# Kernel tuning notes

Hardware: AMD Instinct MI355X
Metric: run time of the kernel (lower is better)

Reference implementation:

```python
import jax, jax.numpy as jnp
import numpy as np

B, N = 4, 8192
D = 128
DEPTH = 4
LEAF = 32
HEADS = 4
HD = D // HEADS
SLOTS = 24
RANKS = [20, 32, 52, 82]                      # rank at encoder step j (fine -> coarse)
EXP = [RANKS[j] * (2 ** j) for j in range(DEPTH)]  # HODLR head output dims


def _rope_tables(seq_len, dim):
    inv_freq = 1.0 / (10000.0 ** (jnp.arange(0, dim, 2, dtype=jnp.float32) / dim))
    t = jnp.arange(seq_len, dtype=jnp.float32)
    freqs = t[:, None] * inv_freq[None, :]
    emb = jnp.concatenate([freqs, freqs], axis=-1)   # [S, dim]
    return jnp.cos(emb), jnp.sin(emb)


def _rotate_half(x):
    x1, x2 = jnp.split(x, 2, axis=-1)
    return jnp.concatenate([-x2, x1], axis=-1)


def _layernorm(x, g, b, eps=1e-5):
    mu = jnp.mean(x, -1, keepdims=True)
    var = jnp.mean((x - mu) ** 2, -1, keepdims=True)
    return (x - mu) * jax.lax.rsqrt(var + eps) * g + b


def _block_attn(h, qkv_w, qkv_b, pw, pb, cos, sin):
    Bc, Nc, C = h.shape
    nb = Nc // LEAF
    xb = h.reshape(Bc * nb, LEAF, C)
    qkv = (xb @ qkv_w + qkv_b).reshape(Bc * nb, LEAF, 3, HEADS, HD)
    qkv = qkv.transpose(2, 0, 3, 1, 4)               # [3, BN, H, L, hd]
    q, k, v = qkv[0], qkv[1], qkv[2]
    q = q * cos + _rotate_half(q) * sin              # full-dim RoPE (rope_dim == head_dim)
    k = k * cos + _rotate_half(k) * sin
    attn = jax.nn.softmax(jnp.einsum('bhqd,bhkd->bhqk', q, k) * (HD ** -0.5), axis=-1)
    o = jnp.einsum('bhqk,bhkd->bhqd', attn, v).transpose(0, 2, 1, 3).reshape(Bc * nb, LEAF, C)
    return (o @ pw + pb).reshape(Bc, Nc, C)


def _forward(x, cen_w, cen_b, nbr_w, nbr_b, inp_w, inp_b,
             leafp_w, leafp_b, leafh_w, leafh_b, log_scale_leaf,
             ln1_g, ln1_b, qkv_w, qkv_b, attnp_w, attnp_b,
             ln2_g, ln2_b, mlp1_w, mlp1_b, mlp2_w, mlp2_b, ds_w, ds_b,
             hu_w0, hu_b0, hv_w0, hv_b0, hu_w1, hu_b1, hv_w1, hv_b1,
             hu_w2, hu_b2, hv_w2, hv_b2, hu_w3, hu_b3, hv_w3, hv_b3):
    Bx, Nx, _ = x.shape
    # --- SymmetricNeighborEmbed (24 neighbor slots, vectorized) ---
    pos_i = x[..., 0:3]
    diag_i = x[..., 3:4]
    h_center = jnp.concatenate([pos_i, diag_i], -1) @ cen_w + cen_b          # [B,N,D]
    nb_feat = x[..., 4:4 + 5 * SLOTS].reshape(Bx, Nx, SLOTS, 5)
    rel = nb_feat[..., 0:1]
    pos_j = nb_feat[..., 1:4]
    w_ij = nb_feat[..., 4:5]
    active = (w_ij != 0.0).astype(x.dtype)
    feat = jnp.concatenate([rel * active, (pos_j - pos_i[:, :, None, :]) * active, w_ij], -1)
    e = (feat @ nbr_w + nbr_b) * active                                       # [B,N,24,D]
    h = h_center + jnp.sum(e, axis=2)
    h = h @ inp_w + inp_b
    # --- leaf dense diagonal blocks ---
    nl = Nx // LEAF
    hl = h.reshape(Bx, nl, LEAF, D) @ leafp_w + leafp_b                       # [B,nl,32,32]
    u_leaf = hl @ leafh_w + leafh_b
    dense = jnp.einsum('blik,bljk->blij', u_leaf, u_leaf) * jnp.exp(log_scale_leaf)
    diag_a = x[..., 3]                                                        # scale_A defaults to 1.0
    mask = jnp.abs(diag_a) > 1e-6
    new_diag = jnp.where(mask, 1.0 / jnp.where(mask, diag_a, 1.0), 1.0).reshape(Bx, nl, LEAF)
    dense = dense + new_diag[..., :, None] * jnp.eye(LEAF, dtype=x.dtype)
    # --- down-only encoder: transformer block -> HODLR head -> 2:1 downsample ---
    cos, sin = _rope_tables(LEAF, HD)
    hu = [(hu_w0, hu_b0), (hu_w1, hu_b1), (hu_w2, hu_b2), (hu_w3, hu_b3)]
    hv = [(hv_w0, hv_b0), (hv_w1, hv_b1), (hv_w2, hv_b2), (hv_w3, hv_b3)]
    us, vs = [], []
    for j in range(DEPTH):
        a = _block_attn(_layernorm(h, ln1_g[j], ln1_b[j]),
                        qkv_w[j], qkv_b[j], attnp_w[j], attnp_b[j], cos, sin)
        h = h + a
        m = _layernorm(h, ln2_g[j], ln2_b[j])
        m = jax.nn.gelu(m @ mlp1_w[j] + mlp1_b[j], approximate=False) @ mlp2_w[j] + mlp2_b[j]
        h = h + m
        us.append((h @ hu[j][0] + hu[j][1]).reshape(Bx, Nx, RANKS[j]))
        vs.append((h @ hv[j][0] + hv[j][1]).reshape(Bx, Nx, RANKS[j]))
        Bh, n, c = h.shape
        h = h.reshape(Bh, n // 2, 2 * c) @ ds_w[j] + ds_b[j]
    # single flat output: dense leaf blocks + all U/V HODLR factors
    return jnp.concatenate([dense.reshape(Bx, -1),
                            jnp.concatenate(us, -1).reshape(Bx, -1),
                            jnp.concatenate(vs, -1).reshape(Bx, -1)], -1)


def setup_inputs():
    key = jax.random.key(0)
    ks = iter(jax.random.split(key, 64))
    def rn(shape, s=0.05):
        return jax.random.normal(next(ks), shape, jnp.float32) * s
    z = lambda *s: jnp.zeros(s, jnp.float32)
    o = lambda *s: jnp.ones(s, jnp.float32)
    inp = {
        'x': jax.random.normal(next(ks), (B, N, 4 + 5 * SLOTS), jnp.float32),
        'cen_w': rn((4, D)), 'cen_b': z(D),
        'nbr_w': rn((5, D)), 'nbr_b': z(D),
        'inp_w': rn((D, D)), 'inp_b': z(D),
        'leafp_w': rn((D, LEAF)), 'leafp_b': z(LEAF),
        'leafh_w': rn((LEAF, LEAF), 0.01), 'leafh_b': z(LEAF),
        'log_scale_leaf': jnp.full((1,), np.log(0.01), jnp.float32),
        'ln1_g': o(DEPTH, D), 'ln1_b': z(DEPTH, D),
        'qkv_w': rn((DEPTH, D, 3 * D)), 'qkv_b': z(DEPTH, 3 * D),
        'attnp_w': rn((DEPTH, D, D)), 'attnp_b': z(DEPTH, D),
        'ln2_g': o(DEPTH, D), 'ln2_b': z(DEPTH, D),
        'mlp1_w': rn((DEPTH, D, 4 * D)), 'mlp1_b': z(DEPTH, 4 * D),
        'mlp2_w': rn((DEPTH, 4 * D, D)), 'mlp2_b': z(DEPTH, D),
        'ds_w': rn((DEPTH, 2 * D, D)), 'ds_b': z(DEPTH, D),
    }
    for j in range(DEPTH):
        inp['hu_w%d' % j] = rn((D, EXP[j]), 0.01)
        inp['hu_b%d' % j] = z(EXP[j])
        inp['hv_w%d' % j] = rn((D, EXP[j]), 0.01)
        inp['hv_b%d' % j] = z(EXP[j])
    return inp


def reference(x, cen_w, cen_b, nbr_w, nbr_b, inp_w, inp_b,
              leafp_w, leafp_b, leafh_w, leafh_b, log_scale_leaf,
              ln1_g, ln1_b, qkv_w, qkv_b, attnp_w, attnp_b,
              ln2_g, ln2_b, mlp1_w, mlp1_b, mlp2_w, mlp2_b, ds_w, ds_b,
              hu_w0, hu_b0, hv_w0, hv_b0, hu_w1, hu_b1, hv_w1, hv_b1,
              hu_w2, hu_b2, hv_w2, hv_b2, hu_w3, hu_b3, hv_w3, hv_b3):
    return _forward(x, cen_w, cen_b, nbr_w, nbr_b, inp_w, inp_b,
                    leafp_w, leafp_b, leafh_w, leafh_b, log_scale_leaf,
                    ln1_g, ln1_b, qkv_w, qkv_b, attnp_w, attnp_b,
                    ln2_g, ln2_b, mlp1_w, mlp1_b, mlp2_w, mlp2_b, ds_w, ds_b,
                    hu_w0, hu_b0, hv_w0, hv_b0, hu_w1, hu_b1, hv_w1, hv_b1,
                    hu_w2, hu_b2, hv_w2, hv_b2, hu_w3, hu_b3, hv_w3, hv_b3)
```

## Files before the change

kernel.cpp:

```cpp
#include <hip/hip_runtime.h>
#include <math.h>

#define DEV __device__ __forceinline__

constexpr int XFv = 124;
constexpr size_t OPB   = 3309568;
constexpr size_t UBASE = 262144;
constexpr size_t VBASE = 1785856;
constexpr int UVWID = 186;

using bfrag  = __attribute__((ext_vector_type(8))) short;
using f32x4v = __attribute__((ext_vector_type(4))) float;

DEV float* at4p(float* base, int t, int c0, int W) {
  return base + t * W + ((c0 + 4 * t) & (W - 1));
}
DEV float& at1r(float* base, int t, int c, int W) {
  return base[t * W + (((c & ~3) + 4 * t) & (W - 1)) + (c & 3)];
}
DEV float4 ld4g(const float* p) { return *(const float4*)p; }
DEV void fma4(float4& a, float s, const float4& w) {
  a.x += s * w.x; a.y += s * w.y; a.z += s * w.z; a.w += s * w.w;
}
DEV float gelu_fast(float x) {
// ... 157 lines not shown
  int t = tid & 31, cg = tid >> 5;
  {
    float4 acc = ld4g(&lpb[4 * cg]);
    for (int k4 = 0; k4 < 128; k4 += 4) {
      float4 xv = *(const float4*)at4p(HS, t, k4, 128);
      float xa[4] = {xv.x, xv.y, xv.z, xv.w};
#pragma unroll
      for (int kk = 0; kk < 4; kk++)
        fma4(acc, xa[kk], ld4g(&lpw[(k4 + kk) * 32 + 4 * cg]));
    }
    *(float4*)at4p(HL, t, 4 * cg, 32) = acc;
  }
  __syncthreads();
  {
    float4 acc = ld4g(&lhb[4 * cg]);
    for (int k4 = 0; k4 < 32; k4 += 4) {
      float4 xv = *(const float4*)at4p(HL, t, k4, 32);
      float xa[4] = {xv.x, xv.y, xv.z, xv.w};
#pragma unroll
      for (int kk = 0; kk < 4; kk++)
        fma4(acc, xa[kk], ld4g(&lhw[(k4 + kk) * 32 + 4 * cg]));
    }
    *(float4*)at4p(UL, t, 4 * cg, 32) = acc;
  }
  __syncthreads();
  {
    float scale = expf(lsc[0]);
    float acc[4] = {0.f, 0.f, 0.f, 0.f};
    for (int k4 = 0; k4 < 32; k4 += 4) {
      float4 xv = *(const float4*)at4p(UL, t, k4, 32);
      float xa[4] = {xv.x, xv.y, xv.z, xv.w};
#pragma unroll
      for (int kk = 0; kk < 4; kk++) {
        int k = k4 + kk;
#pragma unroll
        for (int i2 = 0; i2 < 4; i2++)
          acc[i2] += xa[kk] * at1r(UL, 4 * cg + i2, k, 32);
      }
    }
    int b = leaf >> 8, l = leaf & 255;
#pragma unroll
    for (int i2 = 0; i2 < 4; i2++) {
      int c = 4 * cg + i2;
      float v = acc[i2] * scale;
      if (c == t) {
        float dg = x[(size_t)(leaf * 32 + t) * XFv + 3];
        v += (fabsf(dg) > 1e-6f) ? (1.0f / dg) : 1.0f;
      }
      out[(size_t)b * OPB + (size_t)l * 1024 + t * 32 + c] = v;
    }
  }
}

__global__ __launch_bounds__(256, 4) void layer_mfma_kernel(
    float* __restrict__ h,
    const float* __restrict__ lng, const float* __restrict__ lnb,
    const ushort* __restrict__ wqkvt, const float* __restrict__ bqkv,
    const ushort* __restrict__ wpt, const float* __restrict__ pb,
    const float* __restrict__ rt,
    const float* __restrict__ ln2g, const float* __restrict__ ln2b,
    const ushort* __restrict__ w1t, const float* __restrict__ b1,
    const ushort* __restrict__ w2t, const float* __restrict__ b2) {
  __shared__ __align__(16) ushort SM[16384];
  ushort* XN = SM;
  ushort* QB = SM + 4096;
  ushort* KB = SM + 8192;
  ushort* VT = SM + 12288;
  float*  HS = (float*)(SM + 8192);
  int tid = threadIdx.x;
  size_t base = (size_t)blockIdx.x * (32 * 128);

  {
    int m = tid >> 3, p = tid & 7;
    const float* row = h + base + m * 128 + p * 16;
    float v[16];
    float s = 0.f;
#pragma unroll
    for (int i = 0; i < 16; i += 4) {
      float4 t4 = ld4g(row + i);
      v[i] = t4.x; v[i + 1] = t4.y; v[i + 2] = t4.z; v[i + 3] = t4.w;
      s += t4.x + t4.y + t4.z + t4.w;
    }
    s += __shfl_xor(s, 1); s += __shfl_xor(s, 2); s += __shfl_xor(s, 4);
    float mu = s * (1.0f / 128.0f);
    float s2 = 0.f;
#pragma unroll
    for (int i = 0; i < 16; i++) { float d = v[i] - mu; s2 += d * d; }
    s2 += __shfl_xor(s2, 1); s2 += __shfl_xor(s2, 2); s2 += __shfl_xor(s2, 4);
    float rs = rsqrtf(s2 * (1.0f / 128.0f) + 1e-5f);
    unsigned* XW = (unsigned*)XN;
#pragma unroll
    for (int i = 0; i < 16; i += 2) {
      int c = p * 16 + i;
      float x0 = (v[i] - mu) * rs * lng[c] + lnb[c];
      float x1 = (v[i + 1] - mu) * rs * lng[c + 1] + lnb[c + 1];
      int kp = c >> 1;
      XW[m * 64 + ((kp + 4 * m) & 63)] =
          (unsigned)f2bf(x0) | ((unsigned)f2bf(x1) << 16);
    }
  }
  __syncthreads();

  int w = tid >> 6, l = tid & 63, lm = l & 15, q = l >> 4;

  {
    f32x4v acc[2][6];
#pragma unroll
    for (int mt = 0; mt < 2; mt++)
#pragma unroll
      for (int nt = 0; nt < 6; nt++) acc[mt][nt] = (f32x4v){0.f, 0.f, 0.f, 0.f};
    for (int ks = 0; ks < 4; ks++) {
      bfrag a[2];
#pragma unroll
      for (int mt = 0; mt < 2; mt++) {
        int mm = mt * 16 + lm;
// ... 96 lines not shown
          int qt = mt2 * 16 + q * 4 + r;
          int kc = nt2 * 16 + lm;
          SP[head * 1024 + qt * 32 + (((kc & ~7) + 8 * qt) & 31) + (kc & 7)] =
              f2bf(sc[mt2][nt2][r] * scl);
        }
  }
  __syncthreads();

  {
    if (tid < 128) {
      int head = tid >> 5, qt = tid & 31;
      ushort* rowp = SP + head * 1024 + qt * 32;
      float v[32];
#pragma unroll
      for (int pc = 0; pc < 4; pc++) {
        uint4 ch = *(const uint4*)&rowp[pc * 8];
        unsigned uu[4] = {ch.x, ch.y, ch.z, ch.w};
#pragma unroll
        for (int i2 = 0; i2 < 4; i2++) {
          v[pc * 8 + 2 * i2]     = __uint_as_float(uu[i2] << 16);
          v[pc * 8 + 2 * i2 + 1] = __uint_as_float(uu[i2] & 0xffff0000u);
        }
      }
      float mx = -1e30f;
#pragma unroll
      for (int i = 0; i < 32; i++) mx = fmaxf(mx, v[i]);
      float s = 0.f;
#pragma unroll
      for (int i = 0; i < 32; i++) { v[i] = __expf(v[i] - mx); s += v[i]; }
      float inv = 1.0f / s;
#pragma unroll
      for (int pc = 0; pc < 4; pc++) {
        uint4 ch;
        unsigned uu[4];
#pragma unroll
        for (int i2 = 0; i2 < 4; i2++)
          uu[i2] = (unsigned)f2bf(v[pc * 8 + 2 * i2] * inv) |
                   ((unsigned)f2bf(v[pc * 8 + 2 * i2 + 1] * inv) << 16);
        ch.x = uu[0]; ch.y = uu[1]; ch.z = uu[2]; ch.w = uu[3];
        *(uint4*)&rowp[pc * 8] = ch;
      }
    }
  }
  __syncthreads();

  ushort* OB = QB;
  {
    int head = w;
    f32x4v ov[2][2];
#pragma unroll
    for (int a2 = 0; a2 < 2; a2++)
#pragma unroll
      for (int b2 = 0; b2 < 2; b2++) ov[a2][b2] = (f32x4v){0.f, 0.f, 0.f, 0.f};
    bfrag pa[2], vb[2];
#pragma unroll
    for (int mt2 = 0; mt2 < 2; mt2++) {
      int qt = mt2 * 16 + lm;
      pa[mt2] = *(const bfrag*)&SP[head * 1024 + qt * 32 + ((q * 8 + 8 * qt) & 31)];
    }
#pragma unroll
    for (int nt2 = 0; nt2 < 2; nt2++) {
      int gdim = head * 32 + nt2 * 16 + lm;
      vb[nt2] = *(const bfrag*)&VT[gdim * 32 + ((q * 8 + 8 * gdim) & 31)];
    }
#pragma unroll
    for (int mt2 = 0; mt2 < 2; mt2++)
#pragma unroll
      for (int nt2 = 0; nt2 < 2; nt2++)
        ov[mt2][nt2] = __builtin_amdgcn_mfma_f32_16x16x32_bf16(
            pa[mt2], vb[nt2], ov[mt2][nt2], 0, 0, 0);
#pragma unroll
    for (int mt2 = 0; mt2 < 2; mt2++)
#pragma unroll
      for (int nt2 = 0; nt2 < 2; nt2++)
#pragma unroll
        for (int r = 0; r < 4; r++) {
          int qt = mt2 * 16 + q * 4 + r;
          int gdim = head * 32 + nt2 * 16 + lm;
          stb128(OB, qt, gdim, ov[mt2][nt2][r]);
        }
  }
  __syncthreads();

  {
    f32x4v po[2][2];
#pragma unroll
    for (int mt = 0; mt < 2; mt++)
#pragma unroll
      for (int nt = 0; nt < 2; nt++) po[mt][nt] = (f32x4v){0.f, 0.f, 0.f, 0.f};
    for (int ks = 0; ks < 4; ks++) {
      bfrag a[2];
#pragma unroll
      for (int mt = 0; mt < 2; mt++) {
        int mm = mt * 16 + lm;
        a[mt] = *(const bfrag*)&OB[mm * 128 + ((ks * 32 + q * 8 + 8 * mm) & 127)];
      }
#pragma unroll
      for (int nt = 0; nt < 2; nt++) {
        int n = w * 32 + nt * 16 + lm;
        bfrag b = *(const bfrag*)&wpt[(size_t)n * 128 + ks * 32 + q * 8];
#pragma unroll
        for (int mt = 0; mt < 2; mt++)
          po[mt][nt] = __builtin_amdgcn_mfma_f32_16x16x32_bf16(
              a[mt], b, po[mt][nt], 0, 0, 0);
      }
    }
#pragma unroll
    for (int nt = 0; nt < 2; nt++) {
      int n = w * 32 + nt * 16 + lm;
      float bv = pb[n];
#pragma unroll
      for (int mt = 0; mt < 2; mt++)
#pragma unroll
        for (int r = 0; r < 4; r++) {
          int mm = mt * 16 + q * 4 + r;
          at1r(HS, mm, n, 128) = po[mt][nt][r] + bv;
        }
    }
  }
  __syncthreads();

  {
    int j = tid & 31;
// ... 58 lines not shown
      for (int nt = 0; nt < 2; nt++) {
        int n = hc * 128 + w * 32 + nt * 16 + lm;
        bfrag b = *(const bfrag*)&w1t[(size_t)n * 128 + ks * 32 + q * 8];
#pragma unroll
        for (int mt = 0; mt < 2; mt++)
          acc1[mt][nt] = __builtin_amdgcn_mfma_f32_16x16x32_bf16(
              a[mt], b, acc1[mt][nt], 0, 0, 0);
      }
    }
    if (hc) __syncthreads();
#pragma unroll
    for (int nt = 0; nt < 2; nt++) {
      int nl = w * 32 + nt * 16 + lm;
      float b1v = b1[hc * 128 + nl];
#pragma unroll
      for (int mt = 0; mt < 2; mt++)
#pragma unroll
        for (int r = 0; r < 4; r++) {
          int mm = mt * 16 + q * 4 + r;
          float val = gelu_fast(acc1[mt][nt][r] + b1v);
          HC[mm * 128 + (((nl & ~7) + 8 * mm) & 127) + (nl & 7)] = f2bf(val);
        }
    }
    __syncthreads();
#pragma unroll
    for (int ks = 0; ks < 4; ks++) {
      bfrag a[2];
#pragma unroll
      for (int mt = 0; mt < 2; mt++) {
        int mm = mt * 16 + lm;
        a[mt] = *(const bfrag*)&HC[mm * 128 + ((ks * 32 + q * 8 + 8 * mm) & 127)];
      }
#pragma unroll
      for (int nt = 0; nt < 2; nt++) {
        int n = w * 32 + nt * 16 + lm;
        bfrag b = *(const bfrag*)&w2t[(size_t)n * 512 + hc * 128 + ks * 32 + q * 8];
#pragma unroll
        for (int mt = 0; mt < 2; mt++)
          acc2[mt][nt] = __builtin_amdgcn_mfma_f32_16x16x32_bf16(
              a[mt], b, acc2[mt][nt], 0, 0, 0);
      }
    }
  }

#pragma unroll
  for (int nt = 0; nt < 2; nt++) {
    int n = w * 32 + nt * 16 + lm;
    float b2v = b2[n];
#pragma unroll
    for (int mt = 0; mt < 2; mt++)
#pragma unroll
      for (int r = 0; r < 4; r++) {
        int mm = mt * 16 + q * 4 + r;
        h[base + (size_t)mm * 128 + n] = at1r(HS, mm, n, 128) + acc2[mt][nt][r] + b2v;
      }
  }
}

template <int EXPJ, int RANK, int LVL, int NSPLIT>
__global__ __launch_bounds__(256) void uv_mfma_kernel(
    const float* __restrict__ h,
    const ushort* __restrict__ uwt, const float* __restrict__ ub,
    const ushort* __restrict__ vwt, const float* __restrict__ vb,
    float* __restrict__ out, int Nj) {
  constexpr int NT16 = (EXPJ + 15) / 16;
  constexpr int NJOBS = 2 * NT16;
  constexpr int COFF = (LVL == 0) ? 0 : (LVL == 1) ? 20 : (LVL == 2) ? 52 : 104;
  __shared__ __align__(16) ushort XN[64 * 128];
  int tid = threadIdx.x;
  int t0 = blockIdx.x * 64;
  size_t base = (size_t)t0 * 128;
  {
    int m = tid >> 2, p = tid & 3;
    const float* row = h + base + m * 128 + p * 32;
    unsigned* XW = (unsigned*)XN;
#pragma unroll
    for (int i = 0; i < 32; i += 4) {
      float4 t4 = ld4g(row + i);
      int kp = (p * 32 + i) >> 1;
      XW[m * 64 + ((kp + 4 * m) & 63)] =
          (unsigned)f2bf(t4.x) | ((unsigned)f2bf(t4.y) << 16);
      XW[m * 64 + ((kp + 1 + 4 * m) & 63)] =
          (unsigned)f2bf(t4.z) | ((unsigned)f2bf(t4.w) << 16);
    }
  }
  __syncthreads();
  int bidx = t0 / Nj;
  int tl0 = t0 - bidx * Nj;
  size_t obase = (size_t)bidx * OPB;
  int w = tid >> 6, l = tid & 63, lm = l & 15, q = l >> 4;
  int gw = w + 4 * blockIdx.y;
  for (int jj = gw; jj < NJOBS; jj += 4 * NSPLIT) {
    int uvsel = jj & 1, nt = jj >> 1;
    const ushort* wt = uvsel ? vwt : uwt;
    const float* bias = uvsel ? vb : ub;
    size_t ob = obase + (uvsel ? VBASE : UBASE);
    f32x4v acc[4];
#pragma unroll
    for (int mt = 0; mt < 4; mt++) acc[mt] = (f32x4v){0.f, 0.f, 0.f, 0.f};
    for (int ks = 0; ks < 4; ks++) {
      bfrag b = *(const bfrag*)&wt[(size_t)(nt * 16 + lm) * 128 + ks * 32 + q * 8];
#pragma unroll
      for (int mt = 0; mt < 4; mt++) {
        int mm = mt * 16 + lm;
        int ke = ks * 32 + q * 8;
        bfrag a = *(const bfrag*)&XN[mm * 128 + ((ke + 8 * mm) & 127)];
        acc[mt] = __builtin_amdgcn_mfma_f32_16x16x32_bf16(a, b, acc[mt], 0, 0, 0);
      }
    }
    int c = nt * 16 + lm;
    if (c < EXPJ) {
      float bv = bias[c];
      int cdiv = c / RANK, cmod = c - cdiv * RANK;
#pragma unroll
      for (int mt = 0; mt < 4; mt++)
#pragma unroll
        for (int r = 0; r < 4; r++) {
          int mm = mt * 16 + q * 4 + r;
          int nrow = ((tl0 + mm) << LVL) + cdiv;
          out[ob + (size_t)nrow * UVWID + COFF + cmod] = acc[mt][r] + bv;
        }
    }
  }
}

__global__ __launch_bounds__(256) void ds_mfma_kernel(
    const float* __restrict__ hin, float* __restrict__ hout,
    const ushort* __restrict__ wt, const float* __restrict__ bias) {
  __shared__ __align__(16) ushort XN[64 * 256];
  int tid = threadIdx.x;
  size_t base = (size_t)blockIdx.x * (64 * 256);
  {
    int m = tid >> 2, p = tid & 3;
    const float* row = hin + base + m * 256 + p * 64;
    unsigned* XW = (unsigned*)XN;
#pragma unroll
    for (int i = 0; i < 64; i += 4) {
      float4 t4 = ld4g(row + i);
      int kp = (p * 64 + i) >> 1;
      XW[m * 128 + ((kp + 4 * m) & 127)] =
          (unsigned)f2bf(t4.x) | ((unsigned)f2bf(t4.y) << 16);
      XW[m * 128 + ((kp + 1 + 4 * m) & 127)] =
          (unsigned)f2bf(t4.z) | ((unsigned)f2bf(t4.w) << 16);
    }
  }
  __syncthreads();
  int w = tid >> 6, l = tid & 63, lm = l & 15, q = l >> 4;
  f32x4v acc[4][2];
#pragma unroll
  for (int mt = 0; mt < 4; mt++)
#pragma unroll
    for (int nt = 0; nt < 2; nt++) acc[mt][nt] = (f32x4v){0.f, 0.f, 0.f, 0.f};
  for (int ks = 0; ks < 8; ks++) {
    bfrag a[4];
#pragma unroll
    for (int mt = 0; mt < 4; mt++) {
      int mm = mt * 16 + lm;
      a[mt] = *(const bfrag*)&XN[mm * 256 + ((ks * 32 + q * 8 + 8 * mm) & 255)];
    }
#pragma unroll
    for (int nt = 0; nt < 2; nt++) {
      int n = w * 32 + nt * 16 + lm;
      bfrag b = *(const bfrag*)&wt[(size_t)n * 256 + ks * 32 + q * 8];
#pragma unroll
      for (int mt = 0; mt < 4; mt++)
        acc[mt][nt] = __builtin_amdgcn_mfma_f32_16x16x32_bf16(
            a[mt], b, acc[mt][nt], 0, 0, 0);
    }
  }
  size_t obase = (size_t)blockIdx.x * (64 * 128);
#pragma unroll
  for (int nt = 0; nt < 2; nt++) {
    int n = w * 32 + nt * 16 + lm;
    float bv = bias[n];
#pragma unroll
    for (int mt = 0; mt < 4; mt++)
#pragma unroll
      for (int r = 0; r < 4; r++) {
        int mm = mt * 16 + q * 4 + r;
        hout[obase + (size_t)mm * 128 + n] = acc[mt][nt][r] + bv;
      }
  }
}

extern "C" void kernel_launch(void* const* d_in, const int* in_sizes, int n_in,
                              void* d_out, int out_size, void* d_ws, size_t ws_size,
                              hipStream_t stream) {
  const float* x       = (const float*)d_in[0];
  const float* cen_w   = (const float*)d_in[1];
  const float* cen_b   = (const float*)d_in[2];
  const float* nbr_w   = (const float*)d_in[3];
  const float* nbr_b   = (const float*)d_in[4];
  const float* inp_w   = (const float*)d_in[5];
  const float* inp_b   = (const float*)d_in[6];
  const float* leafp_w = (const float*)d_in[7];
  const float* leafp_b = (const float*)d_in[8];
  const float* leafh_w = (const float*)d_in[9];
  const float* leafh_b = (const float*)d_in[10];
  const float* lscale  = (const float*)d_in[11];
  const float* ln1_g   = (const float*)d_in[12];
  const float* ln1_b   = (const float*)d_in[13];
  const float* qkv_w   = (const float*)d_in[14];
  const float* qkv_b   = (const float*)d_in[15];
  const float* attnp_w = (const float*)d_in[16];
  const float* attnp_b = (const float*)d_in[17];
  const float* ln2_g   = (const float*)d_in[18];
  const float* ln2_b   = (const float*)d_in[19];
  const float* mlp1_w  = (const float*)d_in[20];
  const float* mlp1_b  = (const float*)d_in[21];
  const float* mlp2_w  = (const float*)d_in[22];
  const float* mlp2_b  = (const float*)d_in[23];
  const float* ds_w    = (const float*)d_in[24];
  const float* ds_b    = (const float*)d_in[25];
  const float* huw[4], *hub[4], *hvw[4], *hvb[4];
  for (int j = 0; j < 4; j++) {
    huw[j] = (const float*)d_in[26 + 4 * j];
    hub[j] = (const float*)d_in[27 + 4 * j];
    hvw[j] = (const float*)d_in[28 + 4 * j];
    hvb[j] = (const float*)d_in[29 + 4 * j];
  }
  float* out = (float*)d_out;
  float* hA = (float*)d_ws;
  float* hB = hA + (size_t)4 * 8192 * 128;
  ushort* w1t = (ushort*)(hB + (size_t)2097152);
  ushort* w2t = w1t + (size_t)4 * 65536;
  ushort* uvt = w2t + (size_t)4 * 65536;
  const int NPAD[4] = {32, 64, 208, 656};
  ushort* uwt[4]; ushort* vwt[4];
  ushort* p = uvt;
  for (int j = 0; j < 4; j++) {
    uwt[j] = p; p += (size_t)NPAD[j] * 128;
    vwt[j] = p; p += (size_t)NPAD[j] * 128;
  }
  ushort* wqkvt = p;
  ushort* wpt   = wqkvt + (size_t)4 * 384 * 128;
  ushort* dswt  = wpt + (size_t)4 * 128 * 128;
  float* weff   = (float*)(dswt + (size_t)4 * 128 * 256);
  float* ropetab = weff + 1408;
  const int EXPJ_[4] = {20, 64, 208, 656};

  weff_prep_kernel<<<1, 128, 0, stream>>>(
      cen_w, cen_b, nbr_w, nbr_b, inp_w, inp_b, weff, ropetab);
  wprep_all_kernel<<<dim3(2, 8, 4), 256, 0, stream>>>(mlp1_w, w1t, 128, 512);
  wprep_all_kernel<<<dim3(8, 2, 4), 256, 0, stream>>>(mlp2_w, w2t, 512, 128);
  wprep_all_kernel<<<dim3(2, 6, 4), 256, 0, stream>>>(qkv_w, wqkvt, 128, 384);
  wprep_all_kernel<<<dim3(2, 2, 4), 256, 0, stream>>>(attnp_w, wpt, 128, 128);
  wprep_all_kernel<<<dim3(4, 2, 4), 256, 0, stream>>>(ds_w, dswt, 256, 128);
  {
    UVDesc d;
    for (int j = 0; j < 4; j++) {
      d.src[2 * j] = huw[j];     d.dst[2 * j] = uwt[j];
      d.src[2 * j + 1] = hvw[j]; d.dst[2 * j + 1] = vwt[j];
      d.expj[2 * j] = EXPJ_[j];  d.expj[2 * j + 1] = EXPJ_[j];
      d.npad[2 * j] = NPAD[j];   d.npad[2 * j + 1] = NPAD[j];
    }
    uvprep_all_kernel<<<dim3(328, 8), 256, 0, stream>>>(d);
  }

  node_embed2_kernel<<<(4 * 8192) / 64, 256, 0, stream>>>(x, weff, hA);
  leaf_dense_kernel<<<(4 * 8192) / 32, 256, 0, stream>>>(
      hA, x, leafp_w, leafp_b, leafh_w, leafh_b, lscale, out);

  float* cur = hA;
  float* nxt = hB;
  int Nj = 8192;
  for (int j = 0; j < 4; j++) {
    int tokens = 4 * Nj;
    layer_mfma_kernel<<<tokens / 32, 256, 0, stream>>>(
        cur, ln1_g + j * 128, ln1_b + j * 128,
        wqkvt + (size_t)j * 49152, qkv_b + j * 384,
        wpt + (size_t)j * 16384, attnp_b + j * 128, ropetab,
        ln2_g + j * 128, ln2_b + j * 128,
        w1t + (size_t)j * 65536, mlp1_b + j * 512,
        w2t + (size_t)j * 65536, mlp2_b + j * 128);
    if (j == 0)
      uv_mfma_kernel<20, 20, 0, 1><<<dim3(tokens / 64, 1), 256, 0, stream>>>(
          cur, uwt[0], hub[0], vwt[0], hvb[0], out, Nj);
    else if (j == 1)
      uv_mfma_kernel<64, 32, 1, 2><<<dim3(tokens / 64, 2), 256, 0, stream>>>(
          cur, uwt[1], hub[1], vwt[1], hvb[1], out, Nj);
    else if (j == 2)
      uv_mfma_kernel<208, 52, 2, 4><<<dim3(tokens / 64, 4), 256, 0, stream>>>(
          cur, uwt[2], hub[2], vwt[2], hvb[2], out, Nj);
    else
      uv_mfma_kernel<656, 82, 3, 8><<<dim3(tokens / 64, 8), 256, 0, stream>>>(
          cur, uwt[3], hub[3], vwt[3], hvb[3], out, Nj);
    ds_mfma_kernel<<<tokens / 128, 256, 0, stream>>>(
        cur, nxt, dswt + (size_t)j * 32768, ds_b + j * 128);
    float* tmp = cur; cur = nxt; nxt = tmp;
    Nj >>= 1;
  }
  (void)in_sizes; (void)n_in; (void)out_size; (void)ws_size;
}
```

Baseline: 444.2 us.

## Fuse HODLR U/V heads and downsample into per-level layer kernel

Merges the per-level U/V head projection and the downsample GEMM into the end of the transformer layer kernel. The layer output stays in shared memory, is converted to bf16 there, and feeds both projections, so the global write and re-read of h and two extra launches per level go away. Launch bounds move from 4 to 5 blocks per SM. The cost is that the last level's 656-wide U/V work is now spread over only 128 blocks with four waves each, which may leave the GPU underused, and the higher occupancy target may cause register spills.

```diff
diff --git a/kernel.cpp b/kernel.cpp
--- a/kernel.cpp
+++ b/kernel.cpp
@@ -233,15 +233,20 @@
   }
 }
 
-__global__ __launch_bounds__(256, 4) void layer_mfma_kernel(
-    float* __restrict__ h,
+template <int EXPJ, int RANK, int LVL>
+__global__ __launch_bounds__(256, 5) void layer_mfma_kernel(
+    const float* __restrict__ h, float* __restrict__ hout,
     const float* __restrict__ lng, const float* __restrict__ lnb,
     const ushort* __restrict__ wqkvt, const float* __restrict__ bqkv,
     const ushort* __restrict__ wpt, const float* __restrict__ pb,
     const float* __restrict__ rt,
     const float* __restrict__ ln2g, const float* __restrict__ ln2b,
     const ushort* __restrict__ w1t, const float* __restrict__ b1,
-    const ushort* __restrict__ w2t, const float* __restrict__ b2) {
+    const ushort* __restrict__ w2t, const float* __restrict__ b2,
+    const ushort* __restrict__ uwt, const float* __restrict__ ub,
+    const ushort* __restrict__ vwt, const float* __restrict__ vb,
+    float* __restrict__ out, int Nj,
+    const ushort* __restrict__ dwt, const float* __restrict__ dsb) {
   __shared__ __align__(16) ushort SM[16384];
   ushort* XN = SM;
   ushort* QB = SM + 4096;
@@ -444,7 +449,7 @@
     for (int a2 = 0; a2 < 2; a2++)
 #pragma unroll
       for (int b2 = 0; b2 < 2; b2++) ov[a2][b2] = (f32x4v){0.f, 0.f, 0.f, 0.f};
-    bfrag pa[2], vb[2];
+    bfrag pa[2], vb2[2];
 #pragma unroll
     for (int mt2 = 0; mt2 < 2; mt2++) {
       int qt = mt2 * 16 + lm;
@@ -453,14 +458,14 @@
 #pragma unroll
     for (int nt2 = 0; nt2 < 2; nt2++) {
       int gdim = head * 32 + nt2 * 16 + lm;
-      vb[nt2] = *(const bfrag*)&VT[gdim * 32 + ((q * 8 + 8 * gdim) & 31)];
+      vb2[nt2] = *(const bfrag*)&VT[gdim * 32 + ((q * 8 + 8 * gdim) & 31)];
     }
 #pragma unroll
     for (int mt2 = 0; mt2 < 2; mt2++)
 #pragma unroll
       for (int nt2 = 0; nt2 < 2; nt2++)
         ov[mt2][nt2] = __builtin_amdgcn_mfma_f32_16x16x32_bf16(
-            pa[mt2], vb[nt2], ov[mt2][nt2], 0, 0, 0);
+            pa[mt2], vb2[nt2], ov[mt2][nt2], 0, 0, 0);
 #pragma unroll
     for (int mt2 = 0; mt2 < 2; mt2++)
 #pragma unroll
@@ -625,134 +630,96 @@
 #pragma unroll
       for (int r = 0; r < 4; r++) {
         int mm = mt * 16 + q * 4 + r;
-        h[base + (size_t)mm * 128 + n] = at1r(HS, mm, n, 128) + acc2[mt][nt][r] + b2v;
-      }
-  }
-}
-
-template <int EXPJ, int RANK, int LVL, int NSPLIT>
-__global__ __launch_bounds__(256) void uv_mfma_kernel(
-    const float* __restrict__ h,
-    const ushort* __restrict__ uwt, const float* __restrict__ ub,
-    const ushort* __restrict__ vwt, const float* __restrict__ vb,
-    float* __restrict__ out, int Nj) {
-  constexpr int NT16 = (EXPJ + 15) / 16;
-  constexpr int NJOBS = 2 * NT16;
-  constexpr int COFF = (LVL == 0) ? 0 : (LVL == 1) ? 20 : (LVL == 2) ? 52 : 104;
-  __shared__ __align__(16) ushort XN[64 * 128];
-  int tid = threadIdx.x;
-  int t0 = blockIdx.x * 64;
-  size_t base = (size_t)t0 * 128;
-  {
-    int m = tid >> 2, p = tid & 3;
-    const float* row = h + base + m * 128 + p * 32;
+        at1r(HS, mm, n, 128) += acc2[mt][nt][r] + b2v;
+      }
+  }
+  __syncthreads();
+
+  {
+    int j = tid & 31;
     unsigned* XW = (unsigned*)XN;
 #pragma unroll
-    for (int i = 0; i < 32; i += 4) {
-      float4 t4 = ld4g(row + i);
-      int kp = (p * 32 + i) >> 1;
-      XW[m * 64 + ((kp + 4 * m) & 63)] =
-          (unsigned)f2bf(t4.x) | ((unsigned)f2bf(t4.y) << 16);
-      XW[m * 64 + ((kp + 1 + 4 * m) & 63)] =
-          (unsigned)f2bf(t4.z) | ((unsigned)f2bf(t4.w) << 16);
-    }
-  }
-  __syncthreads();
-  int bidx = t0 / Nj;
-  int tl0 = t0 - bidx * Nj;
-  size_t obase = (size_t)bidx * OPB;
-  int w = tid >> 6, l = tid & 63, lm = l & 15, q = l >> 4;
-  int gw = w + 4 * blockIdx.y;
-  for (int jj = gw; jj < NJOBS; jj += 4 * NSPLIT) {
-    int uvsel = jj & 1, nt = jj >> 1;
-    const ushort* wt = uvsel ? vwt : uwt;
-    const float* bias = uvsel ? vb : ub;
-    size_t ob = obase + (uvsel ? VBASE : UBASE);
-    f32x4v acc[4];
-#pragma unroll
-    for (int mt = 0; mt < 4; mt++) acc[mt] = (f32x4v){0.f, 0.f, 0.f, 0.f};
-    for (int ks = 0; ks < 4; ks++) {
-      bfrag b = *(const bfrag*)&wt[(size_t)(nt * 16 + lm) * 128 + ks * 32 + q * 8];
-#pragma unroll
-      for (int mt = 0; mt < 4; mt++) {
-        int mm = mt * 16 + lm;
-        int ke = ks * 32 + q * 8;
-        bfrag a = *(const bfrag*)&XN[mm * 128 + ((ke + 8 * mm) & 127)];
-        acc[mt] = __builtin_amdgcn_mfma_f32_16x16x32_bf16(a, b, acc[mt], 0, 0, 0);
-      }
-    }
-    int c = nt * 16 + lm;
-    if (c < EXPJ) {
-      float bv = bias[c];
-      int cdiv = c / RANK, cmod = c - cdiv * RANK;
-#pragma unroll
-      for (int mt = 0; mt < 4; mt++)
-#pragma unroll
-        for (int r = 0; r < 4; r++) {
-          int mm = mt * 16 + q * 4 + r;
-          int nrow = ((tl0 + mm) << LVL) + cdiv;
-          out[ob + (size_t)nrow * UVWID + COFF + cmod] = acc[mt][r] + bv;
+    for (int k2 = 0; k2 < 4; k2++) {
+      int idx = tid + 256 * k2;
+      int tok = idx >> 5;
+      float4 hv = *(const float4*)at4p(HS, tok, 4 * j, 128);
+      int kp = 2 * j;
+      XW[tok * 64 + ((kp + 4 * tok) & 63)] =
+          (unsigned)f2bf(hv.x) | ((unsigned)f2bf(hv.y) << 16);
+      XW[tok * 64 + ((kp + 1 + 4 * tok) & 63)] =
+          (unsigned)f2bf(hv.z) | ((unsigned)f2bf(hv.w) << 16);
+    }
+  }
+  __syncthreads();
+
+  {
+    constexpr int NT16 = (EXPJ + 15) / 16;
+    constexpr int NJOBS = 2 * NT16;
+    constexpr int COFF = (LVL == 0) ? 0 : (LVL == 1) ? 20 : (LVL == 2) ? 52 : 104;
+    int t0 = blockIdx.x * 32;
+    int bidx = t0 / Nj;
+    int tl0 = t0 - bidx * Nj;
+    size_t obase = (size_t)bidx * OPB;
+    for (int jj = w; jj < NJOBS; jj += 4) {
+      int uvsel = jj & 1, nt = jj >> 1;
+      const ushort* wt = uvsel ? vwt : uwt;
+      const float* bias = uvsel ? vb : ub;
+      size_t ob = obase + (uvsel ? VBASE : UBASE);
+      f32x4v acc[2];
+      acc[0] = (f32x4v){0.f, 0.f, 0.f, 0.f};
+      acc[1] = (f32x4v){0.f, 0.f, 0.f, 0.f};
+      for (int ks = 0; ks < 4; ks++) {
+        bfrag b = *(const bfrag*)&wt[(size_t)(nt * 16 + lm) * 128 + ks * 32 + q * 8];
+#pragma unroll
+        for (int mt = 0; mt < 2; mt++) {
+          int mm = mt * 16 + lm;
+          int ke = ks * 32 + q * 8;
+          bfrag a = *(const bfrag*)&XN[mm * 128 + ((ke + 8 * mm) & 127)];
+          acc[mt] = __builtin_amdgcn_mfma_f32_16x16x32_bf16(a, b, acc[mt], 0, 0, 0);
         }
-    }
-  }
-}
-
-__global__ __launch_bounds__(256) void ds_mfma_kernel(
-    const float* __restrict__ hin, float* __restrict__ hout,
-    const ushort* __restrict__ wt, const float* __restrict__ bias) {
-  __shared__ __align__(16) ushort XN[64 * 256];
-  int tid = threadIdx.x;
-  size_t base = (size_t)blockIdx.x * (64 * 256);
-  {
-    int m = tid >> 2, p = tid & 3;
-    const float* row = hin + base + m * 256 + p * 64;
-    unsigned* XW = (unsigned*)XN;
-#pragma unroll
-    for (int i = 0; i < 64; i += 4) {
-      float4 t4 = ld4g(row + i);
-      int kp = (p * 64 + i) >> 1;
-      XW[m * 128 + ((kp + 4 * m) & 127)] =
-          (unsigned)f2bf(t4.x) | ((unsigned)f2bf(t4.y) << 16);
-      XW[m * 128 + ((kp + 1 + 4 * m) & 127)] =
-          (unsigned)f2bf(t4.z) | ((unsigned)f2bf(t4.w) << 16);
-    }
-  }
-  __syncthreads();
-  int w = tid >> 6, l = tid & 63, lm = l & 15, q = l >> 4;
-  f32x4v acc[4][2];
-#pragma unroll
-  for (int mt = 0; mt < 4; mt++)
-#pragma unroll
-    for (int nt = 0; nt < 2; nt++) acc[mt][nt] = (f32x4v){0.f, 0.f, 0.f, 0.f};
-  for (int ks = 0; ks < 8; ks++) {
-    bfrag a[4];
-#pragma unroll
-    for (int mt = 0; mt < 4; mt++) {
-      int mm = mt * 16 + lm;
-      a[mt] = *(const bfrag*)&XN[mm * 256 + ((ks * 32 + q * 8 + 8 * mm) & 255)];
-    }
+      }
+      int c = nt * 16 + lm;
+      if (c < EXPJ) {
+        float bv = bias[c];
+        int cdiv = c / RANK, cmod = c - cdiv * RANK;
+#pragma unroll
+        for (int mt = 0; mt < 2; mt++)
+#pragma unroll
+          for (int r = 0; r < 4; r++) {
+            int mm = mt * 16 + q * 4 + r;
+            int nrow = ((tl0 + mm) << LVL) + cdiv;
+            out[ob + (size_t)nrow * UVWID + COFF + cmod] = acc[mt][r] + bv;
+          }
+      }
+    }
+  }
+
+  if constexpr (LVL < 3) {
+    f32x4v dacc[2];
+    dacc[0] = (f32x4v){0.f, 0.f, 0.f, 0.f};
+    dacc[1] = (f32x4v){0.f, 0.f, 0.f, 0.f};
+    for (int ks = 0; ks < 8; ks++) {
+      int mm = 2 * lm + (ks >> 2);
+      int col = (ks & 3) * 32 + q * 8;
+      bfrag a = *(const bfrag*)&XN[mm * 128 + ((col + 8 * mm) & 127)];
+#pragma unroll
+      for (int nt = 0; nt < 2; nt++) {
+        int n = w * 32 + nt * 16 + lm;
+        bfrag b = *(const bfrag*)&dwt[(size_t)n * 256 + ks * 32 + q * 8];
+        dacc[nt] = __builtin_amdgcn_mfma_f32_16x16x32_bf16(a, b, dacc[nt], 0, 0, 0);
+      }
+    }
+    size_t obase2 = (size_t)blockIdx.x * (16 * 128);
 #pragma unroll
     for (int nt = 0; nt < 2; nt++) {
       int n = w * 32 + nt * 16 + lm;
-      bfrag b = *(const bfrag*)&wt[(size_t)n * 256 + ks * 32 + q * 8];
-#pragma unroll
-      for (int mt = 0; mt < 4; mt++)
-        acc[mt][nt] = __builtin_amdgcn_mfma_f32_16x16x32_bf16(
-            a[mt], b, acc[mt][nt], 0, 0, 0);
-    }
-  }
-  size_t obase = (size_t)blockIdx.x * (64 * 128);
-#pragma unroll
-  for (int nt = 0; nt < 2; nt++) {
-    int n = w * 32 + nt * 16 + lm;
-    float bv = bias[n];
-#pragma unroll
-    for (int mt = 0; mt < 4; mt++)
+      float bv = dsb[n];
 #pragma unroll
       for (int r = 0; r < 4; r++) {
-        int mm = mt * 16 + q * 4 + r;
-        hout[obase + (size_t)mm * 128 + n] = acc[mt][nt][r] + bv;
-      }
+        int mm = q * 4 + r;
+        hout[obase2 + (size_t)mm * 128 + n] = dacc[nt][r] + bv;
+      }
+    }
   }
 }
 
@@ -836,32 +803,27 @@
 
   float* cur = hA;
   float* nxt = hB;
-  int Nj = 8192;
-  for (int j = 0; j < 4; j++) {
-    int tokens = 4 * Nj;
-    layer_mfma_kernel<<<tokens / 32, 256, 0, stream>>>(
-        cur, ln1_g + j * 128, ln1_b + j * 128,
-        wqkvt + (size_t)j * 49152, qkv_b + j * 384,
-        wpt + (size_t)j * 16384, attnp_b + j * 128, ropetab,
-        ln2_g + j * 128, ln2_b + j * 128,
-        w1t + (size_t)j * 65536, mlp1_b + j * 512,
-        w2t + (size_t)j * 65536, mlp2_b + j * 128);
-    if (j == 0)
-      uv_mfma_kernel<20, 20, 0, 1><<<dim3(tokens / 64, 1), 256, 0, stream>>>(
-          cur, uwt[0], hub[0], vwt[0], hvb[0], out, Nj);
-    else if (j == 1)
-      uv_mfma_kernel<64, 32, 1, 2><<<dim3(tokens / 64, 2), 256, 0, stream>>>(
-          cur, uwt[1], hub[1], vwt[1], hvb[1], out, Nj);
-    else if (j == 2)
-      uv_mfma_kernel<208, 52, 2, 4><<<dim3(tokens / 64, 4), 256, 0, stream>>>(
-          cur, uwt[2], hub[2], vwt[2], hvb[2], out, Nj);
-    else
-      uv_mfma_kernel<656, 82, 3, 8><<<dim3(tokens / 64, 8), 256, 0, stream>>>(
-          cur, uwt[3], hub[3], vwt[3], hvb[3], out, Nj);
-    ds_mfma_kernel<<<tokens / 128, 256, 0, stream>>>(
-        cur, nxt, dswt + (size_t)j * 32768, ds_b + j * 128);
-    float* tmp = cur; cur = nxt; nxt = tmp;
-    Nj >>= 1;
-  }
+  layer_mfma_kernel<20, 20, 0><<<32768 / 32, 256, 0, stream>>>(
+      cur, nxt, ln1_g, ln1_b, wqkvt, qkv_b, wpt, attnp_b, ropetab,
+      ln2_g, ln2_b, w1t, mlp1_b, w2t, mlp2_b,
+      uwt[0], hub[0], vwt[0], hvb[0], out, 8192, dswt, ds_b);
+  layer_mfma_kernel<64, 32, 1><<<16384 / 32, 256, 0, stream>>>(
+      nxt, cur, ln1_g + 128, ln1_b + 128, wqkvt + 49152, qkv_b + 384,
+      wpt + 16384, attnp_b + 128, ropetab,
+      ln2_g + 128, ln2_b + 128, w1t + 65536, mlp1_b + 512,
+      w2t + 65536, mlp2_b + 128,
+      uwt[1], hub[1], vwt[1], hvb[1], out, 4096, dswt + 32768, ds_b + 128);
+  layer_mfma_kernel<208, 52, 2><<<8192 / 32, 256, 0, stream>>>(
+      cur, nxt, ln1_g + 256, ln1_b + 256, wqkvt + 98304, qkv_b + 768,
+      wpt + 32768, attnp_b + 256, ropetab,
+      ln2_g + 256, ln2_b + 256, w1t + 131072, mlp1_b + 1024,
+      w2t + 131072, mlp2_b + 256,
+      uwt[2], hub[2], vwt[2], hvb[2], out, 2048, dswt + 65536, ds_b + 256);
+  layer_mfma_kernel<656, 82, 3><<<4096 / 32, 256, 0, stream>>>(
+      nxt, cur, ln1_g + 384, ln1_b + 384, wqkvt + 147456, qkv_b + 1152,
+      wpt + 49152, attnp_b + 384, ropetab,
+      ln2_g + 384, ln2_b + 384, w1t + 196608, mlp1_b + 1536,
+      w2t + 196608, mlp2_b + 384,
+      uwt[3], hub[3], vwt[3], hvb[3], out, 1024, dswt + 98304, ds_b + 384);
   (void)in_sizes; (void)n_in; (void)out_size; (void)ws_size;
 }
```

New measurement: 478.8 us. +7.8%, slower.

## Fuse downsample into UV head kernel and stage UV outputs for coalesced assembly

Applied to the files above, without the earlier changes.

Merges the downsample GEMM into the UV-projection kernel, so each block reuses the bf16 activation tile already in shared memory and one launch per level goes away. UV outputs now go to contiguous per-level staging buffers instead of scattered strided writes into the output. A final assemble kernel gathers them into the interleaved output layout with float2 stores. This adds an extra write and read of all UV data plus one more launch, in exchange for coalesced stores and fewer launches. The last level still issues a DS kernel argument but skips the downsample via constexpr.

```diff
diff --git a/kernel.cpp b/kernel.cpp
--- a/kernel.cpp
+++ b/kernel.cpp
@@ -444,7 +444,7 @@
     for (int a2 = 0; a2 < 2; a2++)
 #pragma unroll
       for (int b2 = 0; b2 < 2; b2++) ov[a2][b2] = (f32x4v){0.f, 0.f, 0.f, 0.f};
-    bfrag pa[2], vb[2];
+    bfrag pa[2], vb2[2];
 #pragma unroll
     for (int mt2 = 0; mt2 < 2; mt2++) {
       int qt = mt2 * 16 + lm;
@@ -453,14 +453,14 @@
 #pragma unroll
     for (int nt2 = 0; nt2 < 2; nt2++) {
       int gdim = head * 32 + nt2 * 16 + lm;
-      vb[nt2] = *(const bfrag*)&VT[gdim * 32 + ((q * 8 + 8 * gdim) & 31)];
+      vb2[nt2] = *(const bfrag*)&VT[gdim * 32 + ((q * 8 + 8 * gdim) & 31)];
     }
 #pragma unroll
     for (int mt2 = 0; mt2 < 2; mt2++)
 #pragma unroll
       for (int nt2 = 0; nt2 < 2; nt2++)
         ov[mt2][nt2] = __builtin_amdgcn_mfma_f32_16x16x32_bf16(
-            pa[mt2], vb[nt2], ov[mt2][nt2], 0, 0, 0);
+            pa[mt2], vb2[nt2], ov[mt2][nt2], 0, 0, 0);
 #pragma unroll
     for (int mt2 = 0; mt2 < 2; mt2++)
 #pragma unroll
@@ -631,14 +631,15 @@
 }
 
 template <int EXPJ, int RANK, int LVL, int NSPLIT>
-__global__ __launch_bounds__(256) void uv_mfma_kernel(
+__global__ __launch_bounds__(256) void uvds_kernel(
     const float* __restrict__ h,
     const ushort* __restrict__ uwt, const float* __restrict__ ub,
     const ushort* __restrict__ vwt, const float* __restrict__ vb,
-    float* __restrict__ out, int Nj) {
+    float* __restrict__ ustg, float* __restrict__ vstg,
+    float* __restrict__ hout,
+    const ushort* __restrict__ dwt, const float* __restrict__ dsb) {
   constexpr int NT16 = (EXPJ + 15) / 16;
   constexpr int NJOBS = 2 * NT16;
-  constexpr int COFF = (LVL == 0) ? 0 : (LVL == 1) ? 20 : (LVL == 2) ? 52 : 104;
   __shared__ __align__(16) ushort XN[64 * 128];
   int tid = threadIdx.x;
   int t0 = blockIdx.x * 64;
@@ -658,16 +659,13 @@
     }
   }
   __syncthreads();
-  int bidx = t0 / Nj;
-  int tl0 = t0 - bidx * Nj;
-  size_t obase = (size_t)bidx * OPB;
   int w = tid >> 6, l = tid & 63, lm = l & 15, q = l >> 4;
   int gw = w + 4 * blockIdx.y;
   for (int jj = gw; jj < NJOBS; jj += 4 * NSPLIT) {
     int uvsel = jj & 1, nt = jj >> 1;
     const ushort* wt = uvsel ? vwt : uwt;
     const float* bias = uvsel ? vb : ub;
-    size_t ob = obase + (uvsel ? VBASE : UBASE);
+    float* stg = uvsel ? vstg : ustg;
     f32x4v acc[4];
 #pragma unroll
     for (int mt = 0; mt < 4; mt++) acc[mt] = (f32x4v){0.f, 0.f, 0.f, 0.f};
@@ -684,75 +682,89 @@
     int c = nt * 16 + lm;
     if (c < EXPJ) {
       float bv = bias[c];
-      int cdiv = c / RANK, cmod = c - cdiv * RANK;
 #pragma unroll
       for (int mt = 0; mt < 4; mt++)
 #pragma unroll
         for (int r = 0; r < 4; r++) {
           int mm = mt * 16 + q * 4 + r;
-          int nrow = ((tl0 + mm) << LVL) + cdiv;
-          out[ob + (size_t)nrow * UVWID + COFF + cmod] = acc[mt][r] + bv;
+          stg[(size_t)(t0 + mm) * EXPJ + c] = acc[mt][r] + bv;
         }
     }
   }
-}
-
-__global__ __launch_bounds__(256) void ds_mfma_kernel(
-    const float* __restrict__ hin, float* __restrict__ hout,
-    const ushort* __restrict__ wt, const float* __restrict__ bias) {
-  __shared__ __align__(16) ushort XN[64 * 256];
+  if constexpr (LVL < 3) {
+    if (blockIdx.y == 0) {
+      f32x4v dacc[2][2];
+#pragma unroll
+      for (int mt = 0; mt < 2; mt++)
+#pragma unroll
+        for (int nt = 0; nt < 2; nt++) dacc[mt][nt] = (f32x4v){0.f, 0.f, 0.f, 0.f};
+      for (int ks = 0; ks < 8; ks++) {
+        bfrag a[2];
+#pragma unroll
+        for (int mt = 0; mt < 2; mt++) {
+          int rr = mt * 16 + lm;
+          int tok = 2 * rr + (ks >> 2);
+          int c2 = (ks & 3) * 32 + q * 8;
+          a[mt] = *(const bfrag*)&XN[tok * 128 + ((c2 + 8 * tok) & 127)];
+        }
+#pragma unroll
+        for (int nt = 0; nt < 2; nt++) {
+          int n = w * 32 + nt * 16 + lm;
+          bfrag b = *(const bfrag*)&dwt[(size_t)n * 256 + ks * 32 + q * 8];
+#pragma unroll
+          for (int mt = 0; mt < 2; mt++)
+            dacc[mt][nt] = __builtin_amdgcn_mfma_f32_16x16x32_bf16(
+                a[mt], b, dacc[mt][nt], 0, 0, 0);
+        }
+      }
+      size_t ob2 = (size_t)blockIdx.x * (32 * 128);
+#pragma unroll
+      for (int nt = 0; nt < 2; nt++) {
+        int n = w * 32 + nt * 16 + lm;
+        float bv = dsb[n];
+#pragma unroll
+        for (int mt = 0; mt < 2; mt++)
+#pragma unroll
+          for (int r = 0; r < 4; r++) {
+            int mm = mt * 16 + q * 4 + r;
+            hout[ob2 + (size_t)mm * 128 + n] = dacc[mt][nt][r] + bv;
+          }
+      }
+    }
+  }
+}
+
+struct StgPtrs { const float* u[4]; const float* v[4]; };
+__global__ __launch_bounds__(256) void uv_assemble_kernel(
+    StgPtrs sp, float* __restrict__ out) {
+  __shared__ unsigned char JL[93];
+  __shared__ unsigned char CM[93];
   int tid = threadIdx.x;
-  size_t base = (size_t)blockIdx.x * (64 * 256);
-  {
-    int m = tid >> 2, p = tid & 3;
-    const float* row = hin + base + m * 256 + p * 64;
-    unsigned* XW = (unsigned*)XN;
-#pragma unroll
-    for (int i = 0; i < 64; i += 4) {
-      float4 t4 = ld4g(row + i);
-      int kp = (p * 64 + i) >> 1;
-      XW[m * 128 + ((kp + 4 * m) & 127)] =
-          (unsigned)f2bf(t4.x) | ((unsigned)f2bf(t4.y) << 16);
-      XW[m * 128 + ((kp + 1 + 4 * m) & 127)] =
-          (unsigned)f2bf(t4.z) | ((unsigned)f2bf(t4.w) << 16);
-    }
-  }
-  __syncthreads();
-  int w = tid >> 6, l = tid & 63, lm = l & 15, q = l >> 4;
-  f32x4v acc[4][2];
-#pragma unroll
-  for (int mt = 0; mt < 4; mt++)
-#pragma unroll
-    for (int nt = 0; nt < 2; nt++) acc[mt][nt] = (f32x4v){0.f, 0.f, 0.f, 0.f};
-  for (int ks = 0; ks < 8; ks++) {
-    bfrag a[4];
-#pragma unroll
-    for (int mt = 0; mt < 4; mt++) {
-      int mm = mt * 16 + lm;
-      a[mt] = *(const bfrag*)&XN[mm * 256 + ((ks * 32 + q * 8 + 8 * mm) & 255)];
-    }
-#pragma unroll
-    for (int nt = 0; nt < 2; nt++) {
-      int n = w * 32 + nt * 16 + lm;
-      bfrag b = *(const bfrag*)&wt[(size_t)n * 256 + ks * 32 + q * 8];
-#pragma unroll
-      for (int mt = 0; mt < 4; mt++)
-        acc[mt][nt] = __builtin_amdgcn_mfma_f32_16x16x32_bf16(
-            a[mt], b, acc[mt][nt], 0, 0, 0);
-    }
-  }
-  size_t obase = (size_t)blockIdx.x * (64 * 128);
-#pragma unroll
-  for (int nt = 0; nt < 2; nt++) {
-    int n = w * 32 + nt * 16 + lm;
-    float bv = bias[n];
-#pragma unroll
-    for (int mt = 0; mt < 4; mt++)
-#pragma unroll
-      for (int r = 0; r < 4; r++) {
-        int mm = mt * 16 + q * 4 + r;
-        hout[obase + (size_t)mm * 128 + n] = acc[mt][nt][r] + bv;
-      }
+  if (tid < 93) {
+    int c = 2 * tid;
+    int j = (c < 20) ? 0 : (c < 52) ? 1 : (c < 104) ? 2 : 3;
+    int coff = (j == 0) ? 0 : (j == 1) ? 20 : (j == 2) ? 52 : 104;
+    JL[tid] = (unsigned char)j;
+    CM[tid] = (unsigned char)(c - coff);
+  }
+  __syncthreads();
+  int g0 = blockIdx.x * 32;
+  for (int i = tid; i < 32 * 93; i += 256) {
+    int rr = i / 93, cp = i - rr * 93;
+    int g = g0 + rr;
+    int b = g >> 13, n = g & 8191;
+    int j = JL[cp], cm = CM[cp];
+    int expj, rank;
+    if (j == 0)      { expj = 20;  rank = 20; }
+    else if (j == 1) { expj = 64;  rank = 32; }
+    else if (j == 2) { expj = 208; rank = 52; }
+    else             { expj = 656; rank = 82; }
+    int tok = (b << (13 - j)) + (n >> j);
+    int cdiv = n & ((1 << j) - 1);
+    size_t si = (size_t)tok * expj + cdiv * rank + cm;
+    size_t ob = (size_t)b * OPB + (size_t)n * UVWID + 2 * cp;
+    *(float2*)&out[ob + UBASE] = *(const float2*)&sp.u[j][si];
+    *(float2*)&out[ob + VBASE] = *(const float2*)&sp.v[j][si];
   }
 }
 
@@ -810,6 +822,13 @@
   ushort* dswt  = wpt + (size_t)4 * 128 * 128;
   float* weff   = (float*)(dswt + (size_t)4 * 128 * 256);
   float* ropetab = weff + 1408;
+  const size_t STG[4] = {32768ull * 20, 16384ull * 64, 8192ull * 208, 4096ull * 656};
+  float* ustg[4]; float* vstg[4];
+  float* sp2 = ropetab + 1024;
+  for (int j = 0; j < 4; j++) {
+    ustg[j] = sp2; sp2 += STG[j];
+    vstg[j] = sp2; sp2 += STG[j];
+  }
   const int EXPJ_[4] = {20, 64, 208, 656};
 
   weff_prep_kernel<<<1, 128, 0, stream>>>(
@@ -834,34 +853,44 @@
   leaf_dense_kernel<<<(4 * 8192) / 32, 256, 0, stream>>>(
       hA, x, leafp_w, leafp_b, leafh_w, leafh_b, lscale, out);
 
-  float* cur = hA;
-  float* nxt = hB;
-  int Nj = 8192;
-  for (int j = 0; j < 4; j++) {
-    int tokens = 4 * Nj;
-    layer_mfma_kernel<<<tokens / 32, 256, 0, stream>>>(
-        cur, ln1_g + j * 128, ln1_b + j * 128,
-        wqkvt + (size_t)j * 49152, qkv_b + j * 384,
-        wpt + (size_t)j * 16384, attnp_b + j * 128, ropetab,
-        ln2_g + j * 128, ln2_b + j * 128,
-        w1t + (size_t)j * 65536, mlp1_b + j * 512,
-        w2t + (size_t)j * 65536, mlp2_b + j * 128);
-    if (j == 0)
-      uv_mfma_kernel<20, 20, 0, 1><<<dim3(tokens / 64, 1), 256, 0, stream>>>(
-          cur, uwt[0], hub[0], vwt[0], hvb[0], out, Nj);
-    else if (j == 1)
-      uv_mfma_kernel<64, 32, 1, 2><<<dim3(tokens / 64, 2), 256, 0, stream>>>(
-          cur, uwt[1], hub[1], vwt[1], hvb[1], out, Nj);
-    else if (j == 2)
-      uv_mfma_kernel<208, 52, 2, 4><<<dim3(tokens / 64, 4), 256, 0, stream>>>(
-          cur, uwt[2], hub[2], vwt[2], hvb[2], out, Nj);
-    else
-      uv_mfma_kernel<656, 82, 3, 8><<<dim3(tokens / 64, 8), 256, 0, stream>>>(
-          cur, uwt[3], hub[3], vwt[3], hvb[3], out, Nj);
-    ds_mfma_kernel<<<tokens / 128, 256, 0, stream>>>(
-        cur, nxt, dswt + (size_t)j * 32768, ds_b + j * 128);
-    float* tmp = cur; cur = nxt; nxt = tmp;
-    Nj >>= 1;
+  layer_mfma_kernel<<<32768 / 32, 256, 0, stream>>>(
+      hA, ln1_g, ln1_b, wqkvt, qkv_b, wpt, attnp_b, ropetab,
+      ln2_g, ln2_b, w1t, mlp1_b, w2t, mlp2_b);
+  uvds_kernel<20, 20, 0, 1><<<dim3(512, 1), 256, 0, stream>>>(
+      hA, uwt[0], hub[0], vwt[0], hvb[0], ustg[0], vstg[0],
+      hB, dswt, ds_b);
+
+  layer_mfma_kernel<<<16384 / 32, 256, 0, stream>>>(
+      hB, ln1_g + 128, ln1_b + 128, wqkvt + 49152, qkv_b + 384,
+      wpt + 16384, attnp_b + 128, ropetab,
+      ln2_g + 128, ln2_b + 128, w1t + 65536, mlp1_b + 512,
+      w2t + 65536, mlp2_b + 128);
+  uvds_kernel<64, 32, 1, 2><<<dim3(256, 2), 256, 0, stream>>>(
+      hB, uwt[1], hub[1], vwt[1], hvb[1], ustg[1], vstg[1],
+      hA, dswt + 32768, ds_b + 128);
+
+  layer_mfma_kernel<<<8192 / 32, 256, 0, stream>>>(
+      hA, ln1_g + 256, ln1_b + 256, wqkvt + 98304, qkv_b + 768,
+      wpt + 32768, attnp_b + 256, ropetab,
+      ln2_g + 256, ln2_b + 256, w1t + 131072, mlp1_b + 1024,
+      w2t + 131072, mlp2_b + 256);
+  uvds_kernel<208, 52, 2, 4><<<dim3(128, 4), 256, 0, stream>>>(
+      hA, uwt[2], hub[2], vwt[2], hvb[2], ustg[2], vstg[2],
+      hB, dswt + 65536, ds_b + 256);
+
+  layer_mfma_kernel<<<4096 / 32, 256, 0, stream>>>(
+      hB, ln1_g + 384, ln1_b + 384, wqkvt + 147456, qkv_b + 1152,
+      wpt + 49152, attnp_b + 384, ropetab,
+      ln2_g + 384, ln2_b + 384, w1t + 196608, mlp1_b + 1536,
+      w2t + 196608, mlp2_b + 384);
+  uvds_kernel<656, 82, 3, 8><<<dim3(64, 8), 256, 0, stream>>>(
+      hB, uwt[3], hub[3], vwt[3], hvb[3], ustg[3], vstg[3],
+      hA , dswt , ds_b );
+
+  {
+    StgPtrs sp;
+    for (int j = 0; j < 4; j++) { sp.u[j] = ustg[j]; sp.v[j] = vstg[j]; }
+    uv_assemble_kernel<<<32768 / 32, 256, 0, stream>>>(sp, out);
   }
   (void)in_sizes; (void)n_in; (void)out_size; (void)ws_size;
 }
```

Measured after the change: 441.0 us. No clear change (-0.7%).
